# Performance work log

Hardware: AMD Instinct MI355X
Metric: run time of the kernel (lower is better)

Reference implementation:

```python
import jax, jax.numpy as jnp
import numpy as np

HIDDEN = 2048
HEADS = 16
HEAD_DIM = HIDDEN // HEADS
ROPE_THETA = 10000.0


def setup_inputs() -> dict:
    key = jax.random.key(0)
    ks = jax.random.split(key, 5)
    B, S = 2, 2048
    hidden_states = jax.random.normal(ks[0], (B, S, HIDDEN), dtype=jnp.float32)
    position_ids = jnp.broadcast_to(jnp.arange(S, dtype=jnp.int64), (B, S))
    # Linear params (torch Linear: y = x @ W.T + b); store as [in, out]
    sc = 1.0 / np.sqrt(HIDDEN)
    Wqkv = jax.random.uniform(ks[1], (HIDDEN, 3 * HIDDEN), jnp.float32, -sc, sc)
    bqkv = jax.random.uniform(ks[2], (3 * HIDDEN,), jnp.float32, -sc, sc)
    Wo = jax.random.uniform(ks[3], (HIDDEN, HIDDEN), jnp.float32, -sc, sc)
    bo = jax.random.uniform(ks[4], (HIDDEN,), jnp.float32, -sc, sc)
    return {"hidden_states": hidden_states, "position_ids": position_ids,
            "Wqkv": Wqkv, "bqkv": bqkv, "Wo": Wo, "bo": bo}


def _rotate_half(x):
    x1, x2 = jnp.split(x, 2, axis=-1)
    return jnp.concatenate([-x2, x1], axis=-1)


def _rope_cos_sin(position_ids):
    # inv_freq: [Dh/2]
    inv_freq = 1.0 / (ROPE_THETA ** (jnp.arange(0, HEAD_DIM, 2, dtype=jnp.float32) / HEAD_DIM))
    ang = position_ids.astype(jnp.float32)[..., None] * inv_freq  # [B,S,Dh/2]
    emb = jnp.concatenate([ang, ang], axis=-1)  # [B,S,Dh]
    return jnp.cos(emb)[:, None], jnp.sin(emb)[:, None]  # [B,1,S,Dh]


def reference(hidden_states, position_ids, Wqkv, bqkv, Wo, bo):
    B, S, _ = hidden_states.shape
    qkv = hidden_states @ Wqkv + bqkv  # [B,S,3*H*Dh]
    qkv = qkv.reshape(B, S, 3, HEADS, HEAD_DIM).transpose(2, 0, 3, 1, 4)
    q, k, v = qkv[0], qkv[1], qkv[2]  # each [B,H,S,Dh]
    cos, sin = _rope_cos_sin(position_ids)
    q = q * cos + _rotate_half(q) * sin
    k = k * cos + _rotate_half(k) * sin
    scale = HEAD_DIM ** -0.5
    scores = jnp.einsum('bhqd,bhkd->bhqk', q, k) * scale
    mask = jnp.triu(jnp.full((S, S), -jnp.inf, dtype=scores.dtype), k=1)
    attn = jax.nn.softmax(scores + mask, axis=-1)
    out = jnp.einsum('bhqk,bhkd->bhqd', attn, v)
    out = out.transpose(0, 2, 1, 3).reshape(B, S, HIDDEN)
    return out @ Wo + bo
```

## Files before the change

### kernel.cpp

```cpp
#include <hip/hip_runtime.h>
#include <stdint.h>

typedef __attribute__((ext_vector_type(8))) short bf16x8;
typedef __attribute__((ext_vector_type(4))) float f32x4;

__device__ __forceinline__ float bf2f(ushort u) {
  union { uint32_t u; float f; } v; v.u = ((uint32_t)u) << 16; return v.f;
}
__device__ __forceinline__ ushort f2bf(float f) {
  union { float f; uint32_t u; } v; v.f = f;
  uint32_t r = (v.u + 0x7fffu + ((v.u >> 16) & 1u)) >> 16;
  return (ushort)r;
}

__device__ __forceinline__ f32x4 mfma16(bf16x8 a, bf16x8 b, f32x4 c) {
  return __builtin_amdgcn_mfma_f32_16x16x32_bf16(a, b, c, 0, 0, 0);
}

__device__ __forceinline__ void glds16(const ushort* g, ushort* l) {
  __builtin_amdgcn_global_load_lds(
      (__attribute__((address_space(1))) void*)(void*)g,
      (__attribute__((address_space(3))) void*)(void*)l, 16, 0, 0);
}

__global__ __launch_bounds__(256) void cast_f32_bf16(
    const float* __restrict__ in, ushort* __restrict__ out, long n) {
  const long i = ((long)blockIdx.x * 256 + threadIdx.x) * 4;
  if (i + 3 >= n) {
    for (long j = i; j < n; j++) out[j] = f2bf(in[j]);
    return;
  }
  const float4 v = *(const float4*)&in[i];
  ushort4 o;
  o.x = f2bf(v.x); o.y = f2bf(v.y); o.z = f2bf(v.z); o.w = f2bf(v.w);
  *(ushort4*)&out[i] = o;
}

__global__ __launch_bounds__(256) void transpose_cast(
    const float* __restrict__ in, ushort* __restrict__ out, int R, int C) {
  __shared__ ushort t[32][33];
  const int tx = threadIdx.x & 31, ty = threadIdx.x >> 5;
  const int bc = blockIdx.x * 32;
  const int br = blockIdx.y * 32;
#pragma unroll
  for (int i = 0; i < 32; i += 8)
    t[ty + i][tx] = f2bf(in[(long)(br + ty + i) * C + bc + tx]);
  __syncthreads();
#pragma unroll
  for (int i = 0; i < 32; i += 8)
    out[(long)(bc + ty + i) * R + br + tx] = t[tx][ty + i];
}

template <bool F32OUT>
__global__ __launch_bounds__(256) void gemm_bt_bias(
    const ushort* __restrict__ A, const ushort* __restrict__ Bt,
    const float* __restrict__ bias, void* __restrict__ Cout,
    int M, int N, int K) {
  __shared__ ushort As[128 * 32];
  __shared__ ushort Bs[128 * 32];
  const int tid = threadIdx.x;
  const int wave = tid >> 6;
  const int lane = tid & 63;
  const int quad = lane >> 4;
  const int l16 = lane & 15;
  const int bm = blockIdx.x * 128;
  const int bn = blockIdx.y * 128;
  const int wr = (wave >> 1) * 64;
  const int wc = (wave & 1) * 64;

  f32x4 acc[4][4] = {};

  const long arow = bm + wave * 16 + (lane >> 2);
  const long brow = bn + wave * 16 + (lane >> 2);
  const int kcol = (lane & 3) * 8;
  const ushort* Ag = A + arow * K + kcol;
  const ushort* Bg = Bt + brow * K + kcol;
  ushort* AsW = &As[wave * 512];
  ushort* BsW = &Bs[wave * 512];

  for (int k0 = 0; k0 < K; k0 += 32) {
    __syncthreads();
    glds16(Ag + k0, AsW);
    glds16(Ag + k0 + (long)64 * K, AsW + 64 * 32);
    glds16(Bg + k0, BsW);
    glds16(Bg + k0 + (long)64 * K, BsW + 64 * 32);
    __syncthreads();

    bf16x8 af[4], bfr[4];
#pragma unroll
    for (int i = 0; i < 4; i++)
      af[i] = *(const bf16x8*)&As[(wr + i * 16 + l16) * 32 + quad * 8];
#pragma unroll
    for (int j = 0; j < 4; j++)
      bfr[j] = *(const bf16x8*)&Bs[(wc + j * 16 + l16) * 32 + quad * 8];
#pragma unroll
    for (int i = 0; i < 4; i++)
#pragma unroll
      for (int j = 0; j < 4; j++)
        acc[i][j] = mfma16(af[i], bfr[j], acc[i][j]);
  }

#pragma unroll
  for (int i = 0; i < 4; i++) {
#pragma unroll
    for (int j = 0; j < 4; j++) {
      const int col = bn + wc + j * 16 + l16;
      const float bv = bias[col];
#pragma unroll
      for (int r = 0; r < 4; r++) {
        const int row = bm + wr + i * 16 + quad * 4 + r;
        const float v = acc[i][j][r] + bv;
        if (F32OUT)
          ((float*)Cout)[(long)row * N + col] = v;
        else
          ((ushort*)Cout)[(long)row * N + col] = f2bf(v);
      }
    }
  }
}

__global__ __launch_bounds__(256) void rope_table(float* __restrict__ tab) {
  const int i = blockIdx.x * 256 + threadIdx.x;
  const int d = i & 63, s = i >> 6;
  const float f = powf(10000.0f, -(float)(2 * d) / 128.0f);
  const float ang = (float)s * f;
  tab[i] = cosf(ang);
  tab[131072 + i] = sinf(ang);
}

__global__ __launch_bounds__(256) void rope_apply(ushort* __restrict__ qkv,
                                                  const float* __restrict__ tab) {
  const int idx = blockIdx.x * 256 + threadIdx.x;
  const int d = idx & 63;
  const int h = (idx >> 6) & 15;
  const long bs = idx >> 10;
  const int s = (int)(bs & 2047);
  const float c = tab[(s << 6) + d];
  const float sn = tab[131072 + (s << 6) + d];
  ushort* row = qkv + bs * 6144 + h * 128;
  {
    float x1 = bf2f(row[d]), x2 = bf2f(row[d + 64]);
    row[d] = f2bf(x1 * c - x2 * sn);
    row[d + 64] = f2bf(x2 * c + x1 * sn);
  }
  {
    ushort* rk = row + 2048;
    float x1 = bf2f(rk[d]), x2 = bf2f(rk[d + 64]);
    rk[d] = f2bf(x1 * c - x2 * sn);
    rk[d + 64] = f2bf(x2 * c + x1 * sn);
  }
}

#define KSTR 136
#define VSTR 68
__global__ __launch_bounds__(256) void attn_part(
    const ushort* __restrict__ qkv, float* __restrict__ part_o,
    float* __restrict__ part_l, int T, int slots_bh) {
  const int S = 2048, LD = 6144;
  const int tid = threadIdx.x;
  const int wave = tid >> 6, lane = tid & 63;
  const int quad = lane >> 4, l16 = lane & 15;
  const int h = blockIdx.y;
  const int b = blockIdx.z;

  int y = blockIdx.x, qt = -1, ch = 0;
  for (int q = 31; q >= 0; --q) {
    const int c = q / T + 1;
    if (qt < 0) {
      if (y < c) { qt = q; ch = y; } else y -= c;
    }
  }
  int sb = 0;
  for (int q = 0; q < qt; q++) sb += q / T + 1;
  const long slot = ((long)(b * 16 + h)) * slots_bh + sb + ch;

  const ushort* base = qkv + (long)b * S * LD;
  const int qrow0 = qt * 64 + wave * 16;
  const int kb0 = ch * T * 64;
  const int kbend = min((ch + 1) * T * 64, qt * 64 + 64);

  __shared__ ushort Ks[64 * KSTR];
  __shared__ ushort Vs[128 * VSTR];
  __shared__ ushort Ps[4][16 * VSTR];

  bf16x8 qf[4];
  {
    const ushort* qp = base + (long)(qrow0 + l16) * LD + h * 128 + quad * 8;
#pragma unroll
    for (int c = 0; c < 4; c++) qf[c] = *(const bf16x8*)(qp + c * 32);
  }

  float l_lane[4] = {0.f, 0.f, 0.f, 0.f};
  f32x4 o[8];
#pragma unroll
  for (int f = 0; f < 8; f++) o[f] = (f32x4){0.f, 0.f, 0.f, 0.f};

  const float scale = 0.08838834764831845f;

  const int k_row = tid >> 4;
  const int k_dcol = (tid & 15) * 8;
  const int v_key2 = (tid & 31) * 2;
  const int v_dc0 = tid >> 5;

  for (int kb = kb0; kb < kbend; kb += 64) {
    __syncthreads();
#pragma unroll
    for (int it = 0; it < 4; it++) {
      const int row = k_row + it * 16;
      *(uint4*)&Ks[row * KSTR + k_dcol] =
          *(const uint4*)(base + (long)(kb + row) * LD + 2048 + h * 128 + k_dcol);
    }
#pragma unroll
    for (int it = 0; it < 2; it++) {
      const int dc = v_dc0 + it * 8;
      const ushort* vg = base + (long)(kb + v_key2) * LD + 4096 + h * 128 + dc * 8;
      ushort va[8] __attribute__((aligned(16)));
      ushort vb[8] __attribute__((aligned(16)));
      *(uint4*)va = *(const uint4*)vg;
      *(uint4*)vb = *(const uint4*)(vg + LD);
#pragma unroll
      for (int e = 0; e < 8; e++) {
        const uint32_t pk = (uint32_t)va[e] | ((uint32_t)vb[e] << 16);
        *(uint32_t*)&Vs[(dc * 8 + e) * VSTR + v_key2] = pk;
      }
    }
    __syncthreads();

    int nkt = (qrow0 + 15 - kb) / 16 + 1;
    if (nkt > 4) nkt = 4;

    f32x4 sc[4] = {};
#pragma unroll
    for (int kt = 0; kt < 4; kt++) {
      if (kt < nkt) {
#pragma unroll
        for (int c = 0; c < 4; c++) {
          bf16x8 kf = *(const bf16x8*)&Ks[(kt * 16 + l16) * KSTR + c * 32 + quad * 8];
          sc[kt] = mfma16(qf[c], kf, sc[kt]);
        }
      }
    }

#pragma unroll
    for (int r = 0; r < 4; r++) {
      const int qpos = qrow0 + quad * 4 + r;
      const int prow = (quad * 4 + r) * VSTR;
      float psum = 0.f;
#pragma unroll
      for (int kt = 0; kt < 4; kt++) {
        const float e = __expf(sc[kt][r] * scale);
        const float p = (kb + kt * 16 + l16 > qpos) ? 0.f : e;
        psum += p;
        Ps[wave][prow + kt * 16 + l16] = f2bf(p);
      }
      l_lane[r] += psum;
    }

    bf16x8 pf0 = *(const bf16x8*)&Ps[wave][l16 * VSTR + quad * 8];
#pragma unroll
    for (int f = 0; f < 8; f++) {
      bf16x8 vf0 = *(const bf16x8*)&Vs[(f * 16 + l16) * VSTR + quad * 8];
      o[f] = mfma16(pf0, vf0, o[f]);
    }
    if (nkt > 2) {
      bf16x8 pf1 = *(const bf16x8*)&Ps[wave][l16 * VSTR + 32 + quad * 8];
#pragma unroll
      for (int f = 0; f < 8; f++) {
        bf16x8 vf1 = *(const bf16x8*)&Vs[(f * 16 + l16) * VSTR + 32 + quad * 8];
        o[f] = mfma16(pf1, vf1, o[f]);
      }
    }
  }

  float* po = part_o + slot * 8192;
#pragma unroll
  for (int r = 0; r < 4; r++) {
    float l = l_lane[r];
    l += __shfl_xor(l, 1);
    l += __shfl_xor(l, 2);
    l += __shfl_xor(l, 4);
    l += __shfl_xor(l, 8);
    const int row = wave * 16 + quad * 4 + r;
#pragma unroll
    for (int f = 0; f < 8; f++)
      po[row * 128 + f * 16 + l16] = o[f][r];
    if (l16 == 0) part_l[slot * 64 + row] = l;
  }
}

__global__ __launch_bounds__(256) void attn_merge(
    const float* __restrict__ part_o, const float* __restrict__ part_l,
    ushort* __restrict__ attnb, int T, int slots_bh) {
  const int qt = blockIdx.x, h = blockIdx.y, b = blockIdx.z;
  const int tid = threadIdx.x;
  const int cnt = qt / T + 1;
  int sb = 0;
  for (int q = 0; q < qt; q++) sb += q / T + 1;
  const long slot0 = ((long)(b * 16 + h)) * slots_bh + sb;

  for (int e4 = tid; e4 < 2048; e4 += 256) {
    const int elem = e4 * 4;
    const int row = elem >> 7;
    const int d = elem & 127;
    float4 s = {0.f, 0.f, 0.f, 0.f};
    float l = 0.f;
    for (int c = 0; c < cnt; c++) {
      const float4 p = *(const float4*)&part_o[(slot0 + c) * 8192 + elem];
      s.x += p.x; s.y += p.y; s.z += p.z; s.w += p.w;
      l += part_l[(slot0 + c) * 64 + row];
    }
    const float inv = 1.0f / l;
    ushort4 ov;
    ov.x = f2bf(s.x * inv); ov.y = f2bf(s.y * inv);
    ov.z = f2bf(s.z * inv); ov.w = f2bf(s.w * inv);
    *(ushort4*)&attnb[((long)b * 2048 + qt * 64 + row) * 2048 + h * 128 + d] = ov;
  }
}

static const void* find_by_size(void* const* d_in, const int* in_sizes,
                                int n_in, long want) {
  for (int i = 0; i < n_in; i++)
    if ((long)in_sizes[i] == want) return d_in[i];
  return nullptr;
}

extern "C" void kernel_launch(void* const* d_in, const int* in_sizes, int n_in,
                              void* d_out, int out_size, void* d_ws, size_t ws_size,
                              hipStream_t stream) {
  const float* hidden = (const float*)find_by_size(d_in, in_sizes, n_in, 8388608);
  const float* Wqkv   = (const float*)find_by_size(d_in, in_sizes, n_in, 12582912);
  const float* bqkv   = (const float*)find_by_size(d_in, in_sizes, n_in, 6144);
  const float* Wo     = (const float*)find_by_size(d_in, in_sizes, n_in, 4194304);
  const float* bo     = (const float*)find_by_size(d_in, in_sizes, n_in, 2048);

  uintptr_t w = (uintptr_t)d_ws;
  ushort* hiddenB = (ushort*)w; w += (size_t)4096 * 2048 * 2;
  ushort* WqkvT   = (ushort*)w; w += (size_t)6144 * 2048 * 2;
  ushort* WoT     = (ushort*)w; w += (size_t)2048 * 2048 * 2;
  ushort* qkvb    = (ushort*)w; w += (size_t)4096 * 6144 * 2;
  ushort* attnb   = (ushort*)w; w += (size_t)4096 * 2048 * 2;
  float*  tab     = (float*)w;  w += (size_t)2048 * 64 * 2 * 4;
  const size_t fixed_bytes = w - (uintptr_t)d_ws;

  int T = 8, slots_bh = 0;
  for (;; T *= 2) {
    slots_bh = 0;
    for (int q = 0; q < 32; q++) slots_bh += q / T + 1;
    const size_t need = fixed_bytes +
        (size_t)slots_bh * 32 * (8192 + 64) * 4;
    if (need <= ws_size || T >= 32) break;
  }
  float* part_o = (float*)w; w += (size_t)slots_bh * 32 * 8192 * 4;
  float* part_l = (float*)w; w += (size_t)slots_bh * 32 * 64 * 4;

  cast_f32_bf16<<<8192, 256, 0, stream>>>(hidden, hiddenB, 8388608L);
  transpose_cast<<<dim3(192, 64), 256, 0, stream>>>(Wqkv, WqkvT, 2048, 6144);
  transpose_cast<<<dim3(64, 64), 256, 0, stream>>>(Wo, WoT, 2048, 2048);
  rope_table<<<512, 256, 0, stream>>>(tab);
  gemm_bt_bias<false><<<dim3(32, 48), 256, 0, stream>>>(hiddenB, WqkvT, bqkv,
                                                        qkvb, 4096, 6144, 2048);
  rope_apply<<<16384, 256, 0, stream>>>(qkvb, tab);
  attn_part<<<dim3(slots_bh, 16, 2), 256, 0, stream>>>(qkvb, part_o, part_l,
                                                       T, slots_bh);
  attn_merge<<<dim3(32, 16, 2), 256, 0, stream>>>(part_o, part_l, attnb,
                                                  T, slots_bh);
  gemm_bt_bias<true><<<dim3(32, 16), 256, 0, stream>>>(attnb, WoT, bo,
                                                       d_out, 4096, 2048, 2048);
}
```

Baseline: 460.9 us.

## Replace GEMMs with 256x256 double-buffered pipelined MFMA kernel

Replaces the simple 128x128 single-buffered GEMM with a 512-thread 256x256 tile kernel that uses K=64 steps, double-buffered LDS with an XOR swizzle, and global-to-LDS loads issued between MFMA quarter-blocks under explicit barriers and waitcnts. It also remaps workgroup IDs for L2 locality and raises MFMA wave priority. The aim is to hide memory latency and raise arithmetic intensity in the QKV and output projections. The cost is higher register and LDS use, and a wave-quantization risk: the output GEMM launches only 128 workgroups.

```diff
diff --git a/kernel.cpp b/kernel.cpp
--- a/kernel.cpp
+++ b/kernel.cpp
@@ -22,6 +22,13 @@
       (__attribute__((address_space(1))) void*)(void*)g,
       (__attribute__((address_space(3))) void*)(void*)l, 16, 0, 0);
 }
+
+#define BAR()  __builtin_amdgcn_s_barrier()
+#define LGK0() asm volatile("s_waitcnt lgkmcnt(0)" ::: "memory")
+#define VMC4() asm volatile("s_waitcnt vmcnt(4)" ::: "memory")
+#define VMC0() asm volatile("s_waitcnt vmcnt(0)" ::: "memory")
+#define PRIO1() __builtin_amdgcn_s_setprio(1)
+#define PRIO0() __builtin_amdgcn_s_setprio(0)
 
 __global__ __launch_bounds__(256) void cast_f32_bf16(
     const float* __restrict__ in, ushort* __restrict__ out, long n) {
@@ -51,64 +58,147 @@
     out[(long)(bc + ty + i) * R + br + tx] = t[tx][ty + i];
 }
 
+
+__device__ __forceinline__ void stg2(const ushort* src, ushort* dst, long kstride) {
+  glds16(src, dst);
+  glds16(src + 64 * kstride, dst + 4096);
+}
+
+__device__ __forceinline__ void rd4(bf16x8 (&d)[4][2], const ushort* p,
+                                    int kq0, int kq1) {
+#pragma unroll
+  for (int ii = 0; ii < 4; ii++) {
+    d[ii][0] = *(const bf16x8*)&p[ii * 1024 + kq0];
+    d[ii][1] = *(const bf16x8*)&p[ii * 1024 + kq1];
+  }
+}
+__device__ __forceinline__ void rd2(bf16x8 (&d)[2][2], const ushort* p,
+                                    int kq0, int kq1) {
+#pragma unroll
+  for (int jj = 0; jj < 2; jj++) {
+    d[jj][0] = *(const bf16x8*)&p[jj * 1024 + kq0];
+    d[jj][1] = *(const bf16x8*)&p[jj * 1024 + kq1];
+  }
+}
+template <int I0, int J0>
+__device__ __forceinline__ void mmq(f32x4 (&acc)[8][4], const bf16x8 (&a)[4][2],
+                                    const bf16x8 (&b)[2][2]) {
+#pragma unroll
+  for (int ii = 0; ii < 4; ii++)
+#pragma unroll
+    for (int jj = 0; jj < 2; jj++)
+#pragma unroll
+      for (int ks = 0; ks < 2; ks++)
+        acc[I0 + ii][J0 + jj] =
+            mfma16(a[ii][ks], b[jj][ks], acc[I0 + ii][J0 + jj]);
+}
+
 template <bool F32OUT>
-__global__ __launch_bounds__(256) void gemm_bt_bias(
+__global__ __launch_bounds__(512, 2) void gemm256(
     const ushort* __restrict__ A, const ushort* __restrict__ Bt,
     const float* __restrict__ bias, void* __restrict__ Cout,
-    int M, int N, int K) {
-  __shared__ ushort As[128 * 32];
-  __shared__ ushort Bs[128 * 32];
+    int N, int K, int NBM) {
+  __shared__ ushort lds[2][2][16384];
   const int tid = threadIdx.x;
-  const int wave = tid >> 6;
-  const int lane = tid & 63;
-  const int quad = lane >> 4;
-  const int l16 = lane & 15;
-  const int bm = blockIdx.x * 128;
-  const int bn = blockIdx.y * 128;
-  const int wr = (wave >> 1) * 64;
-  const int wc = (wave & 1) * 64;
-
-  f32x4 acc[4][4] = {};
-
-  const long arow = bm + wave * 16 + (lane >> 2);
-  const long brow = bn + wave * 16 + (lane >> 2);
-  const int kcol = (lane & 3) * 8;
-  const ushort* Ag = A + arow * K + kcol;
-  const ushort* Bg = Bt + brow * K + kcol;
-  ushort* AsW = &As[wave * 512];
-  ushort* BsW = &Bs[wave * 512];
-
-  for (int k0 = 0; k0 < K; k0 += 32) {
-    __syncthreads();
-    glds16(Ag + k0, AsW);
-    glds16(Ag + k0 + (long)64 * K, AsW + 64 * 32);
-    glds16(Bg + k0, BsW);
-    glds16(Bg + k0 + (long)64 * K, BsW + 64 * 32);
-    __syncthreads();
-
-    bf16x8 af[4], bfr[4];
-#pragma unroll
-    for (int i = 0; i < 4; i++)
-      af[i] = *(const bf16x8*)&As[(wr + i * 16 + l16) * 32 + quad * 8];
-#pragma unroll
-    for (int j = 0; j < 4; j++)
-      bfr[j] = *(const bf16x8*)&Bs[(wc + j * 16 + l16) * 32 + quad * 8];
-#pragma unroll
-    for (int i = 0; i < 4; i++)
-#pragma unroll
-      for (int j = 0; j < 4; j++)
-        acc[i][j] = mfma16(af[i], bfr[j], acc[i][j]);
-  }
-
-#pragma unroll
-  for (int i = 0; i < 4; i++) {
+  const int wave = tid >> 6, lane = tid & 63;
+  const int quad = lane >> 4, l16 = lane & 15;
+  const int wm = wave >> 2, wn = wave & 3;
+  const long Kl = K;
+
+  const int nwg = gridDim.x;
+  const int wg = ((int)blockIdx.x & 7) * (nwg >> 3) + ((int)blockIdx.x >> 3);
+  const int bm = (wg % NBM) * 256;
+  const int bn = (wg / NBM) * 256;
+  const int NT = K >> 6;
+
+  const int srow = (wave << 3) + (lane >> 3);
+  const int kc8 = ((lane & 7) ^ ((lane >> 3) & 7)) << 3;
+  const ushort* Asrc = A + (long)(bm + srow) * Kl + kc8;
+  const ushort* Bsrc = Bt + (long)(bn + srow) * Kl + kc8;
+
+#define STAGE(SRC, BUF, MAT, H, KT)                                       \
+  stg2(SRC + (long)(H) * 128 * Kl + (long)(KT) * 64,                      \
+       &lds[BUF][MAT][(H) * 8192 + (wave << 9)], Kl)
+
+  const int kq0 = (quad ^ (l16 & 7)) << 3;
+  const int kq1 = ((4 | quad) ^ (l16 & 7)) << 3;
+
+  f32x4 acc[8][4] = {};
+
+  STAGE(Asrc, 0, 0, 0, 0); STAGE(Asrc, 0, 0, 1, 0);
+  STAGE(Bsrc, 0, 1, 0, 0); STAGE(Bsrc, 0, 1, 1, 0);
+  STAGE(Bsrc, 1, 1, 0, 1); STAGE(Bsrc, 1, 1, 1, 1);
+  VMC4(); BAR();
+
+  const int NI = NT >> 1;
+#pragma unroll 1
+  for (int t = 0; t < NI; ++t) {
+    const int kb = 2 * t + 1;
+    const int kp0 = (2 * t + 2 < NT) ? 2 * t + 2 : NT - 1;
+    const int kp1 = (2 * t + 3 < NT) ? 2 * t + 3 : NT - 1;
+    bf16x8 a[4][2], b0[2][2], b1[2][2];
+
+    rd4(a, &lds[0][0][(wm * 128 + l16) * 64], kq0, kq1);
+    rd2(b0, &lds[0][1][(wn * 64 + l16) * 64], kq0, kq1);
+    STAGE(Asrc, 1, 0, 0, kb);
+    BAR(); LGK0();
+    PRIO1(); mmq<0, 0>(acc, a, b0); PRIO0();
+    BAR();
+
+    rd2(b1, &lds[0][1][(wn * 64 + 32 + l16) * 64], kq0, kq1);
+    STAGE(Asrc, 1, 0, 1, kb);
+    BAR(); LGK0();
+    PRIO1(); mmq<0, 2>(acc, a, b1); PRIO0();
+    BAR();
+
+    rd4(a, &lds[0][0][(wm * 128 + 64 + l16) * 64], kq0, kq1);
+    STAGE(Bsrc, 0, 1, 0, kp0);
+    BAR(); LGK0();
+    PRIO1(); mmq<4, 0>(acc, a, b0); PRIO0();
+    BAR();
+
+    STAGE(Bsrc, 0, 1, 1, kp0);
+    VMC4();
+    BAR();
+    PRIO1(); mmq<4, 2>(acc, a, b1); PRIO0();
+    BAR();
+
+    rd4(a, &lds[1][0][(wm * 128 + l16) * 64], kq0, kq1);
+    rd2(b0, &lds[1][1][(wn * 64 + l16) * 64], kq0, kq1);
+    STAGE(Asrc, 0, 0, 0, kp0);
+    BAR(); LGK0();
+    PRIO1(); mmq<0, 0>(acc, a, b0); PRIO0();
+    BAR();
+
+    rd2(b1, &lds[1][1][(wn * 64 + 32 + l16) * 64], kq0, kq1);
+    STAGE(Asrc, 0, 0, 1, kp0);
+    BAR(); LGK0();
+    PRIO1(); mmq<0, 2>(acc, a, b1); PRIO0();
+    BAR();
+
+    rd4(a, &lds[1][0][(wm * 128 + 64 + l16) * 64], kq0, kq1);
+    STAGE(Bsrc, 1, 1, 0, kp1);
+    BAR(); LGK0();
+    PRIO1(); mmq<4, 0>(acc, a, b0); PRIO0();
+    BAR();
+
+    STAGE(Bsrc, 1, 1, 1, kp1);
+    VMC4();
+    BAR();
+    PRIO1(); mmq<4, 2>(acc, a, b1); PRIO0();
+    BAR();
+  }
+  VMC0();
+
+#pragma unroll
+  for (int i = 0; i < 8; i++) {
 #pragma unroll
     for (int j = 0; j < 4; j++) {
-      const int col = bn + wc + j * 16 + l16;
+      const int col = bn + wn * 64 + j * 16 + l16;
       const float bv = bias[col];
 #pragma unroll
       for (int r = 0; r < 4; r++) {
-        const int row = bm + wr + i * 16 + quad * 4 + r;
+        const int row = bm + wm * 128 + i * 16 + quad * 4 + r;
         const float v = acc[i][j][r] + bv;
         if (F32OUT)
           ((float*)Cout)[(long)row * N + col] = v;
@@ -117,6 +207,7 @@
       }
     }
   }
+#undef STAGE
 }
 
 __global__ __launch_bounds__(256) void rope_table(float* __restrict__ tab) {
@@ -357,13 +448,13 @@
   transpose_cast<<<dim3(192, 64), 256, 0, stream>>>(Wqkv, WqkvT, 2048, 6144);
   transpose_cast<<<dim3(64, 64), 256, 0, stream>>>(Wo, WoT, 2048, 2048);
   rope_table<<<512, 256, 0, stream>>>(tab);
-  gemm_bt_bias<false><<<dim3(32, 48), 256, 0, stream>>>(hiddenB, WqkvT, bqkv,
-                                                        qkvb, 4096, 6144, 2048);
+  gemm256<false><<<dim3(384), 512, 0, stream>>>(hiddenB, WqkvT, bqkv,
+                                                qkvb, 6144, 2048, 16);
   rope_apply<<<16384, 256, 0, stream>>>(qkvb, tab);
   attn_part<<<dim3(slots_bh, 16, 2), 256, 0, stream>>>(qkvb, part_o, part_l,
                                                        T, slots_bh);
   attn_merge<<<dim3(32, 16, 2), 256, 0, stream>>>(part_o, part_l, attnb,
                                                   T, slots_bh);
-  gemm_bt_bias<true><<<dim3(32, 16), 256, 0, stream>>>(attnb, WoT, bo,
-                                                       d_out, 4096, 2048, 2048);
-}
+  gemm256<true><<<dim3(128), 512, 0, stream>>>(attnb, WoT, bo,
+                                               d_out, 2048, 2048, 16);
+}
```

Result: faster. 440.1 us (-4.5%).
